# Performance work log

Measured on AMD Instinct MI355X. Metric: run time of the kernel, lower is better.

The kernel has to match this reference:

```python
import jax, jax.numpy as jnp
import numpy as np

BATCH, IN_F, OUT_F, BASIS = 64, 512, 512, 8


def _cheb_basis(x):
    # Chebyshev basis T_k(tanh(x)) for k=1..BASIS; x: (b, i) -> (b, i, BASIS)
    theta = jnp.arccos(jnp.clip(jnp.tanh(x), -1.0 + 1e-6, 1.0 - 1e-6))
    ks = jnp.arange(1, BASIS + 1, dtype=x.dtype)
    return jnp.cos(theta[..., None] * ks)


def setup_inputs() -> dict:
    key = jax.random.key(0)
    k1, k2, k3 = jax.random.split(key, 3)
    x = jax.random.normal(k1, (BATCH, IN_F), dtype=jnp.float32)
    # xavier_normal_ on w: std = sqrt(2 / (fan_in + fan_out))
    w = jax.random.normal(k2, (IN_F, OUT_F), dtype=jnp.float32) * np.sqrt(2.0 / (IN_F + OUT_F))
    # normal_(c, 0, 0.1)
    c = jax.random.normal(k3, (IN_F, OUT_F, BASIS), dtype=jnp.float32) * 0.1
    return {"x": x, "w": w, "c": c}


def reference(x, w, c):
    # basis: (b, i, k); contract basis dim with c: (i, o, k) -> (b, i, o)
    basis = _cheb_basis(x)
    s = jnp.einsum("bik,iok->bio", basis, c)
    # residual SiLU(x) broadcast over o, weight by w, reduce over in_features
    out = jnp.einsum("bio,io->bo", jax.nn.silu(x)[:, :, None] + s, w)
    return out
```

## Files before the change

kernel.cpp:

```cpp
#include <hip/hip_runtime.h>

#define BATCH 64
#define IN_F 512
#define OUT_F 512
#define NKS 32
#define ICH 16
#define NNS 16

typedef short short8 __attribute__((ext_vector_type(8)));
typedef float f32x4 __attribute__((ext_vector_type(4)));

static __device__ __forceinline__ unsigned bfpk(float a, float b) {
    unsigned ua = __float_as_uint(a) + 0x8000u;
    unsigned ub = __float_as_uint(b) + 0x8000u;
    return __builtin_amdgcn_perm(ub, ua, 0x07060302u);
}

__global__ __launch_bounds__(256) void kan_prep(const float* __restrict__ x,
                                                short* __restrict__ A_c,
                                                short* __restrict__ A_s) {
    int gid = blockIdx.x * 256 + threadIdx.x;
    int i = gid & (IN_F - 1);
    int b = gid >> 9;
    float xv = x[b * IN_F + i];
    float xc = fminf(fmaxf(xv, -15.f), 15.f);
    float u  = __expf(-xc);
    float sl = __fdividef(xv, 1.0f + u);
    float u2 = u * u;
    float t  = __fdividef(1.0f - u2, 1.0f + u2);
    t = fminf(fmaxf(t, -1.0f + 1e-6f), 1.0f - 1e-6f);
    float t2 = t + t;
    float T1 = t;
    float T2 = fmaf(t2, T1, -1.0f);
    float T3 = fmaf(t2, T2, -T1);
    float T4 = fmaf(t2, T3, -T2);
    float T5 = fmaf(t2, T4, -T3);
    float T6 = fmaf(t2, T5, -T4);
    float T7 = fmaf(t2, T6, -T5);
    float T8 = fmaf(t2, T7, -T6);
    union { short8 v; unsigned u4[4]; } fr;
    fr.u4[0] = bfpk(T1, T2);
    fr.u4[1] = bfpk(T3, T4);
    fr.u4[2] = bfpk(T5, T6);
    fr.u4[3] = bfpk(T7, T8);
    *(short8*)(A_c + ((size_t)i * BATCH + b) * 8) = fr.v;
    A_s[(size_t)b * IN_F + i] = (short)(bfpk(sl, 0.f) & 0xffffu);
}

__global__ __launch_bounds__(256, 2) void kan_mfma(const short* __restrict__ A_c,
                                                   const short* __restrict__ A_s,
                                                   const float* __restrict__ w,
                                                   const float* __restrict__ c,
                                                   float* __restrict__ partial) {
    int nb   = blockIdx.x & (NNS - 1);
    int kb   = blockIdx.x >> 4;
    int lane = threadIdx.x & 63;
    int wid  = threadIdx.x >> 6;
    int m    = lane & 15;
    int quad = lane >> 4;
    int b    = wid * 16 + m;
    int i0   = kb * ICH;

    short8 af[4];
#pragma unroll
    for (int s = 0; s < 4; ++s)
        af[s] = *(const short8*)(A_c + ((size_t)(i0 + s * 4 + quad) * BATCH + b) * 8);
    short8 awf = short8{0, 0, 0, 0, 0, 0, 0, 0};
    if (quad < 2)
        awf = *(const short8*)(A_s + (size_t)b * IN_F + i0 + quad * 8);

#pragma unroll
    for (int nf = 0; nf < 2; ++nf) {
        int o = nb * 32 + nf * 16 + m;
        f32x4 acc = {0.f, 0.f, 0.f, 0.f};
#pragma unroll
        for (int s = 0; s < 4; ++s) {
            int i = i0 + s * 4 + quad;
            const float4* cp = (const float4*)(c + ((size_t)i * OUT_F + o) * 8);
            float4 c0 = cp[0];
            float4 c1 = cp[1];
            float wv = w[(size_t)i * OUT_F + o];
            union { short8 v; unsigned u4[4]; } bf;
            bf.u4[0] = bfpk(wv * c0.x, wv * c0.y);
            bf.u4[1] = bfpk(wv * c0.z, wv * c0.w);
            bf.u4[2] = bfpk(wv * c1.x, wv * c1.y);
            bf.u4[3] = bfpk(wv * c1.z, wv * c1.w);
            acc = __builtin_amdgcn_mfma_f32_16x16x32_bf16(af[s], bf.v, acc, 0, 0, 0);
        }
        union { short8 v; unsigned u4[4]; } bw;
        if (quad < 2) {
            const float* wp = w + (size_t)(i0 + quad * 8) * OUT_F + o;
            bw.u4[0] = bfpk(wp[0 * OUT_F], wp[1 * OUT_F]);
            bw.u4[1] = bfpk(wp[2 * OUT_F], wp[3 * OUT_F]);
            bw.u4[2] = bfpk(wp[4 * OUT_F], wp[5 * OUT_F]);
            bw.u4[3] = bfpk(wp[6 * OUT_F], wp[7 * OUT_F]);
        } else {
            bw.u4[0] = bw.u4[1] = bw.u4[2] = bw.u4[3] = 0u;
        }
        acc = __builtin_amdgcn_mfma_f32_16x16x32_bf16(awf, bw.v, acc, 0, 0, 0);

        float* pp = partial + ((size_t)kb * BATCH + wid * 16 + quad * 4) * OUT_F + o;
#pragma unroll
        for (int r = 0; r < 4; ++r) pp[(size_t)r * OUT_F] = acc[r];
    }
}

__global__ __launch_bounds__(256) void kan_reduce(const float* __restrict__ partial,
                                                  float* __restrict__ out) {
    int g = blockIdx.x * 256 + threadIdx.x;
    float a0 = 0.f, a1 = 0.f, a2 = 0.f, a3 = 0.f;
#pragma unroll
    for (int s = 0; s < NKS; s += 4) {
        a0 += partial[(size_t)(s + 0) * (BATCH * OUT_F) + g];
        a1 += partial[(size_t)(s + 1) * (BATCH * OUT_F) + g];
        a2 += partial[(size_t)(s + 2) * (BATCH * OUT_F) + g];
        a3 += partial[(size_t)(s + 3) * (BATCH * OUT_F) + g];
    }
    out[g] = (a0 + a1) + (a2 + a3);
}

extern "C" void kernel_launch(void* const* d_in, const int* in_sizes, int n_in,
                              void* d_out, int out_size, void* d_ws, size_t ws_size,
                              hipStream_t stream) {
    const float* x = (const float*)d_in[0];
    const float* w = (const float*)d_in[1];
    const float* c = (const float*)d_in[2];
    float* out = (float*)d_out;

    short* A_c = (short*)d_ws;
    short* A_s = A_c + (size_t)IN_F * BATCH * 8;
    float* partial = (float*)((char*)d_ws + 589824);

    kan_prep<<<(BATCH * IN_F) / 256, 256, 0, stream>>>(x, A_c, A_s);
    kan_mfma<<<NKS * NNS, 256, 0, stream>>>(A_c, A_s, w, c, partial);
    kan_reduce<<<(BATCH * OUT_F) / 256, 256, 0, stream>>>(partial, out);
}
```

Before: 71.87 us.

## Fuse Chebyshev basis prep into MFMA kernel and retile over batch

Removes the separate prep kernel by computing tanh-Chebyshev and SiLU features per block into LDS, so features no longer round-trip through global memory. Each wave now covers 16 outputs across all 64 batch rows, with four MFMA accumulators, and the K-chunk shrinks to 8 inputs. This saves a launch and the intermediate traffic, but doubles the number of K splits. The partial buffer and the reduce kernel's reads therefore double, and features are recomputed by each of the 8 N-blocks.

```diff
diff --git a/kernel.cpp b/kernel.cpp
--- a/kernel.cpp
+++ b/kernel.cpp
@@ -3,9 +3,9 @@
 #define BATCH 64
 #define IN_F 512
 #define OUT_F 512
-#define NKS 32
-#define ICH 16
-#define NNS 16
+#define ICH 8
+#define NKS (IN_F / ICH)
+#define NNS 8
 
 typedef short short8 __attribute__((ext_vector_type(8)));
 typedef float f32x4 __attribute__((ext_vector_type(4)));
@@ -16,92 +16,109 @@
     return __builtin_amdgcn_perm(ub, ua, 0x07060302u);
 }
 
-__global__ __launch_bounds__(256) void kan_prep(const float* __restrict__ x,
-                                                short* __restrict__ A_c,
-                                                short* __restrict__ A_s) {
-    int gid = blockIdx.x * 256 + threadIdx.x;
-    int i = gid & (IN_F - 1);
-    int b = gid >> 9;
-    float xv = x[b * IN_F + i];
-    float xc = fminf(fmaxf(xv, -15.f), 15.f);
-    float u  = __expf(-xc);
-    float sl = __fdividef(xv, 1.0f + u);
-    float u2 = u * u;
-    float t  = __fdividef(1.0f - u2, 1.0f + u2);
-    t = fminf(fmaxf(t, -1.0f + 1e-6f), 1.0f - 1e-6f);
-    float t2 = t + t;
-    float T1 = t;
-    float T2 = fmaf(t2, T1, -1.0f);
-    float T3 = fmaf(t2, T2, -T1);
-    float T4 = fmaf(t2, T3, -T2);
-    float T5 = fmaf(t2, T4, -T3);
-    float T6 = fmaf(t2, T5, -T4);
-    float T7 = fmaf(t2, T6, -T5);
-    float T8 = fmaf(t2, T7, -T6);
-    union { short8 v; unsigned u4[4]; } fr;
-    fr.u4[0] = bfpk(T1, T2);
-    fr.u4[1] = bfpk(T3, T4);
-    fr.u4[2] = bfpk(T5, T6);
-    fr.u4[3] = bfpk(T7, T8);
-    *(short8*)(A_c + ((size_t)i * BATCH + b) * 8) = fr.v;
-    A_s[(size_t)b * IN_F + i] = (short)(bfpk(sl, 0.f) & 0xffffu);
-}
-
-__global__ __launch_bounds__(256, 2) void kan_mfma(const short* __restrict__ A_c,
-                                                   const short* __restrict__ A_s,
+__global__ __launch_bounds__(256, 2) void kan_mfma(const float* __restrict__ x,
                                                    const float* __restrict__ w,
                                                    const float* __restrict__ c,
                                                    float* __restrict__ partial) {
-    int nb   = blockIdx.x & (NNS - 1);
-    int kb   = blockIdx.x >> 4;
-    int lane = threadIdx.x & 63;
-    int wid  = threadIdx.x >> 6;
+    __shared__ __align__(16) short T_lds[ICH * BATCH * 8];
+    __shared__ __align__(16) short S_lds[BATCH * 8];
+
+    int nb  = blockIdx.x & (NNS - 1);
+    int kb  = blockIdx.x >> 3;
+    int i0  = kb * ICH;
+    int tid = threadIdx.x;
+
+#pragma unroll
+    for (int h = 0; h < 2; ++h) {
+        int p  = tid + h * 256;
+        int b  = p & 63;
+        int il = p >> 6;
+        float xv = x[(size_t)b * IN_F + i0 + il];
+        float xc = fminf(fmaxf(xv, -15.f), 15.f);
+        float u  = __expf(-xc);
+        float sl = __fdividef(xv, 1.0f + u);
+        float u2 = u * u;
+        float t  = __fdividef(1.0f - u2, 1.0f + u2);
+        t = fminf(fmaxf(t, -1.0f + 1e-6f), 1.0f - 1e-6f);
+        float t2 = t + t;
+        float T1 = t;
+        float T2 = fmaf(t2, T1, -1.0f);
+        float T3 = fmaf(t2, T2, -T1);
+        float T4 = fmaf(t2, T3, -T2);
+        float T5 = fmaf(t2, T4, -T3);
+        float T6 = fmaf(t2, T5, -T4);
+        float T7 = fmaf(t2, T6, -T5);
+        float T8 = fmaf(t2, T7, -T6);
+        union { short8 v; unsigned u4[4]; } fr;
+        fr.u4[0] = bfpk(T1, T2);
+        fr.u4[1] = bfpk(T3, T4);
+        fr.u4[2] = bfpk(T5, T6);
+        fr.u4[3] = bfpk(T7, T8);
+        *(short8*)&T_lds[(il * BATCH + b) * 8] = fr.v;
+        S_lds[b * 8 + il] = (short)(bfpk(sl, 0.f) & 0xffffu);
+    }
+    __syncthreads();
+
+    int lane = tid & 63;
+    int wid  = tid >> 6;
     int m    = lane & 15;
     int quad = lane >> 4;
-    int b    = wid * 16 + m;
-    int i0   = kb * ICH;
+    int o    = nb * 64 + wid * 16 + m;
 
-    short8 af[4];
+    short8 af[4][2];
+    short8 aw[4];
 #pragma unroll
-    for (int s = 0; s < 4; ++s)
-        af[s] = *(const short8*)(A_c + ((size_t)(i0 + s * 4 + quad) * BATCH + b) * 8);
-    short8 awf = short8{0, 0, 0, 0, 0, 0, 0, 0};
-    if (quad < 2)
-        awf = *(const short8*)(A_s + (size_t)b * IN_F + i0 + quad * 8);
+    for (int bt = 0; bt < 4; ++bt) {
+        int b = bt * 16 + m;
+#pragma unroll
+        for (int s = 0; s < 2; ++s)
+            af[bt][s] = *(const short8*)&T_lds[((s * 4 + quad) * BATCH + b) * 8];
+        aw[bt] = (quad == 0) ? *(const short8*)&S_lds[b * 8]
+                             : short8{0, 0, 0, 0, 0, 0, 0, 0};
+    }
+
+    f32x4 acc[4];
+#pragma unroll
+    for (int bt = 0; bt < 4; ++bt) acc[bt] = f32x4{0.f, 0.f, 0.f, 0.f};
 
 #pragma unroll
-    for (int nf = 0; nf < 2; ++nf) {
-        int o = nb * 32 + nf * 16 + m;
-        f32x4 acc = {0.f, 0.f, 0.f, 0.f};
+    for (int s = 0; s < 2; ++s) {
+        int i = i0 + s * 4 + quad;
+        const float4* cp = (const float4*)(c + ((size_t)i * OUT_F + o) * 8);
+        float4 c0 = cp[0];
+        float4 c1 = cp[1];
+        float wv = w[(size_t)i * OUT_F + o];
+        union { short8 v; unsigned u4[4]; } bf;
+        bf.u4[0] = bfpk(wv * c0.x, wv * c0.y);
+        bf.u4[1] = bfpk(wv * c0.z, wv * c0.w);
+        bf.u4[2] = bfpk(wv * c1.x, wv * c1.y);
+        bf.u4[3] = bfpk(wv * c1.z, wv * c1.w);
 #pragma unroll
-        for (int s = 0; s < 4; ++s) {
-            int i = i0 + s * 4 + quad;
-            const float4* cp = (const float4*)(c + ((size_t)i * OUT_F + o) * 8);
-            float4 c0 = cp[0];
-            float4 c1 = cp[1];
-            float wv = w[(size_t)i * OUT_F + o];
-            union { short8 v; unsigned u4[4]; } bf;
-            bf.u4[0] = bfpk(wv * c0.x, wv * c0.y);
-            bf.u4[1] = bfpk(wv * c0.z, wv * c0.w);
-            bf.u4[2] = bfpk(wv * c1.x, wv * c1.y);
-            bf.u4[3] = bfpk(wv * c1.z, wv * c1.w);
-            acc = __builtin_amdgcn_mfma_f32_16x16x32_bf16(af[s], bf.v, acc, 0, 0, 0);
-        }
-        union { short8 v; unsigned u4[4]; } bw;
-        if (quad < 2) {
-            const float* wp = w + (size_t)(i0 + quad * 8) * OUT_F + o;
-            bw.u4[0] = bfpk(wp[0 * OUT_F], wp[1 * OUT_F]);
-            bw.u4[1] = bfpk(wp[2 * OUT_F], wp[3 * OUT_F]);
-            bw.u4[2] = bfpk(wp[4 * OUT_F], wp[5 * OUT_F]);
-            bw.u4[3] = bfpk(wp[6 * OUT_F], wp[7 * OUT_F]);
-        } else {
-            bw.u4[0] = bw.u4[1] = bw.u4[2] = bw.u4[3] = 0u;
-        }
-        acc = __builtin_amdgcn_mfma_f32_16x16x32_bf16(awf, bw.v, acc, 0, 0, 0);
+        for (int bt = 0; bt < 4; ++bt)
+            acc[bt] = __builtin_amdgcn_mfma_f32_16x16x32_bf16(af[bt][s], bf.v,
+                                                              acc[bt], 0, 0, 0);
+    }
 
-        float* pp = partial + ((size_t)kb * BATCH + wid * 16 + quad * 4) * OUT_F + o;
+    union { short8 v; unsigned u4[4]; } bw;
+    if (quad == 0) {
+        const float* wp = w + (size_t)i0 * OUT_F + o;
+        bw.u4[0] = bfpk(wp[0 * OUT_F], wp[1 * OUT_F]);
+        bw.u4[1] = bfpk(wp[2 * OUT_F], wp[3 * OUT_F]);
+        bw.u4[2] = bfpk(wp[4 * OUT_F], wp[5 * OUT_F]);
+        bw.u4[3] = bfpk(wp[6 * OUT_F], wp[7 * OUT_F]);
+    } else {
+        bw.u4[0] = bw.u4[1] = bw.u4[2] = bw.u4[3] = 0u;
+    }
 #pragma unroll
-        for (int r = 0; r < 4; ++r) pp[(size_t)r * OUT_F] = acc[r];
+    for (int bt = 0; bt < 4; ++bt)
+        acc[bt] = __builtin_amdgcn_mfma_f32_16x16x32_bf16(aw[bt], bw.v,
+                                                          acc[bt], 0, 0, 0);
+
+#pragma unroll
+    for (int bt = 0; bt < 4; ++bt) {
+        float* pp = partial + ((size_t)kb * BATCH + bt * 16 + quad * 4) * OUT_F + o;
+#pragma unroll
+        for (int r = 0; r < 4; ++r) pp[(size_t)r * OUT_F] = acc[bt][r];
     }
 }
 
@@ -109,14 +126,19 @@
                                                   float* __restrict__ out) {
     int g = blockIdx.x * 256 + threadIdx.x;
     float a0 = 0.f, a1 = 0.f, a2 = 0.f, a3 = 0.f;
+    float a4 = 0.f, a5 = 0.f, a6 = 0.f, a7 = 0.f;
 #pragma unroll
-    for (int s = 0; s < NKS; s += 4) {
+    for (int s = 0; s < NKS; s += 8) {
         a0 += partial[(size_t)(s + 0) * (BATCH * OUT_F) + g];
         a1 += partial[(size_t)(s + 1) * (BATCH * OUT_F) + g];
         a2 += partial[(size_t)(s + 2) * (BATCH * OUT_F) + g];
         a3 += partial[(size_t)(s + 3) * (BATCH * OUT_F) + g];
+        a4 += partial[(size_t)(s + 4) * (BATCH * OUT_F) + g];
+        a5 += partial[(size_t)(s + 5) * (BATCH * OUT_F) + g];
+        a6 += partial[(size_t)(s + 6) * (BATCH * OUT_F) + g];
+        a7 += partial[(size_t)(s + 7) * (BATCH * OUT_F) + g];
     }
-    out[g] = (a0 + a1) + (a2 + a3);
+    out[g] = ((a0 + a1) + (a2 + a3)) + ((a4 + a5) + (a6 + a7));
 }
 
 extern "C" void kernel_launch(void* const* d_in, const int* in_sizes, int n_in,
@@ -127,11 +149,8 @@
     const float* c = (const float*)d_in[2];
     float* out = (float*)d_out;
 
-    short* A_c = (short*)d_ws;
-    short* A_s = A_c + (size_t)IN_F * BATCH * 8;
-    float* partial = (float*)((char*)d_ws + 589824);
+    float* partial = (float*)d_ws;
 
-    kan_prep<<<(BATCH * IN_F) / 256, 256, 0, stream>>>(x, A_c, A_s);
-    kan_mfma<<<NKS * NNS, 256, 0, stream>>>(A_c, A_s, w, c, partial);
+    kan_mfma<<<NKS * NNS, 256, 0, stream>>>(x, w, c, partial);
     kan_reduce<<<(BATCH * OUT_F) / 256, 256, 0, stream>>>(partial, out);
 }
```

Result: slower. 75.20 us (+4.6%).
